# Performance work log

Measured on AMD Instinct MI355X. Metric: run time of the kernel, lower is better.

Reference implementation:

```python
import jax, jax.numpy as jnp
jax.config.update("jax_enable_x64", True)
import numpy as np

BATCH, N = 8192, 4096
EPS = 1e-6
NR_ITERS = 5  # Newton-Raphson iterations in the gate circuit


def setup_inputs() -> dict:
    key = jax.random.key(0)
    x = jax.random.normal(key, (BATCH, N), dtype=jnp.float32)
    return {"x": x}


def reference(x):
    # Faithful numeric emulation of the bit-pulse FP64 gate circuit.
    # The original encodes each scalar as 32 bit-pulses, widens to FP64,
    # and runs the exact arithmetic below on FP64 values, then narrows
    # back to FP32. We operate on the decoded floats directly.
    x64 = x.astype(jnp.float64)                      # FP32ToFP64Converter
    mean = jnp.mean(x64, axis=-1, keepdims=True)     # sum via FP64 adders / N
    c = x64 - mean                                   # x + (-mean) via sign NOT + adder
    var = jnp.mean(c * c, axis=-1, keepdims=True)    # FP64 squares, summed, / N
    vpe = var + EPS
    # rsqrt via Newton-Raphson, seeded with y0 = 1/(var+eps) (FP64 divider)
    y = 1.0 / vpe
    for _ in range(NR_ITERS):
        y = 0.5 * y * (3.0 - vpe * (y * y))
    out = c * y                                      # normalize
    return out.astype(jnp.float32)                   # FP64ToFP32Converter
```

## Files before the change

### kernel.cpp

```cpp
#include <hip/hip_runtime.h>


#define LN_BATCH 8192
#define LN_N     4096
#define LN_THREADS 256
#define LN_EPS 1e-6

__global__ __launch_bounds__(LN_THREADS)
void spike_layernorm_kernel(const float* __restrict__ x, float* __restrict__ out) {
    const int row  = blockIdx.x;
    const int t    = threadIdx.x;
    const int wave = t >> 6;
    const int lane = t & 63;

    const float4* __restrict__ xr  = reinterpret_cast<const float4*>(x + (size_t)row * LN_N);
    float4* __restrict__       orow = reinterpret_cast<float4*>(out + (size_t)row * LN_N);

    float4 v[4];
#pragma unroll
    for (int i = 0; i < 4; ++i) v[i] = xr[t + i * LN_THREADS];

    double s = 0.0;
#pragma unroll
    for (int i = 0; i < 4; ++i)
        s += (double)v[i].x + (double)v[i].y + (double)v[i].z + (double)v[i].w;

#pragma unroll
    for (int off = 32; off > 0; off >>= 1) s += __shfl_down(s, off, 64);

    __shared__ double red[4];
    __shared__ double bcast[2];
    if (lane == 0) red[wave] = s;
    __syncthreads();
    if (t == 0) {
        double tot = red[0] + red[1] + red[2] + red[3];
        bcast[0] = tot * (1.0 / LN_N);
    }
    __syncthreads();
    const double mean = bcast[0];

    double ss = 0.0;
#pragma unroll
    for (int i = 0; i < 4; ++i) {
        double d;
        d = (double)v[i].x - mean; ss += d * d;
        d = (double)v[i].y - mean; ss += d * d;
        d = (double)v[i].z - mean; ss += d * d;
        d = (double)v[i].w - mean; ss += d * d;
    }
#pragma unroll
    for (int off = 32; off > 0; off >>= 1) ss += __shfl_down(ss, off, 64);

    if (lane == 0) red[wave] = ss;
    __syncthreads();
    if (t == 0) {
        double var = (red[0] + red[1] + red[2] + red[3]) * (1.0 / LN_N);
        double vpe = var + LN_EPS;
        double y = 1.0 / vpe;
#pragma unroll
        for (int it = 0; it < 5; ++it)
            y = 0.5 * y * (3.0 - vpe * (y * y));
        bcast[1] = y;
    }
    __syncthreads();
    const double y = bcast[1];

#pragma unroll
    for (int i = 0; i < 4; ++i) {
        float4 o;
        o.x = (float)(((double)v[i].x - mean) * y);
        o.y = (float)(((double)v[i].y - mean) * y);
        o.z = (float)(((double)v[i].z - mean) * y);
        o.w = (float)(((double)v[i].w - mean) * y);
        orow[t + i * LN_THREADS] = o;
    }
}

extern "C" void kernel_launch(void* const* d_in, const int* in_sizes, int n_in,
                              void* d_out, int out_size, void* d_ws, size_t ws_size,
                              hipStream_t stream) {
    const float* x = (const float*)d_in[0];
    float* out = (float*)d_out;
    spike_layernorm_kernel<<<LN_BATCH, LN_THREADS, 0, stream>>>(x, out);
}
```

Before: 226.2 us.

## Map one wavefront per row with shuffle reductions and nontemporal accesses

Reassigns work so each 64-lane wave owns a whole row and holds 16 float4 values per lane, packing four rows per block. This removes all block-level barriers and shared-memory reductions in favor of xor-shuffle allreduces, and splits the FP64 accumulations into four independent chains. Loads and stores use nontemporal hints to avoid cache pollution on streaming data. The cost is higher register pressure per thread, which may reduce occupancy.

```diff
diff --git a/kernel.cpp b/kernel.cpp
--- a/kernel.cpp
+++ b/kernel.cpp
@@ -3,76 +3,83 @@
 
 #define LN_BATCH 8192
 #define LN_N     4096
-#define LN_THREADS 256
-#define LN_EPS 1e-6
+#define LN_WPB   4
+#define LN_THREADS (LN_WPB * 64)
+#define LN_F4PT  16
+#define LN_EPS   1e-6
+
+typedef float vfloat4 __attribute__((ext_vector_type(4)));
+
+__device__ __forceinline__ double wave_allreduce_add(double s) {
+#pragma unroll
+    for (int off = 1; off < 64; off <<= 1)
+        s += __shfl_xor(s, off, 64);
+    return s;
+}
 
 __global__ __launch_bounds__(LN_THREADS)
 void spike_layernorm_kernel(const float* __restrict__ x, float* __restrict__ out) {
-    const int row  = blockIdx.x;
-    const int t    = threadIdx.x;
-    const int wave = t >> 6;
-    const int lane = t & 63;
+    const int wave = threadIdx.x >> 6;
+    const int lane = threadIdx.x & 63;
+    const int row  = blockIdx.x * LN_WPB + wave;
 
-    const float4* __restrict__ xr  = reinterpret_cast<const float4*>(x + (size_t)row * LN_N);
-    float4* __restrict__       orow = reinterpret_cast<float4*>(out + (size_t)row * LN_N);
+    const vfloat4* __restrict__ xr =
+        reinterpret_cast<const vfloat4*>(x + (size_t)row * LN_N);
+    vfloat4* __restrict__ orow =
+        reinterpret_cast<vfloat4*>(out + (size_t)row * LN_N);
 
-    float4 v[4];
+    vfloat4 v[LN_F4PT];
 #pragma unroll
-    for (int i = 0; i < 4; ++i) v[i] = xr[t + i * LN_THREADS];
+    for (int i = 0; i < LN_F4PT; ++i)
+        v[i] = __builtin_nontemporal_load(&xr[lane + i * 64]);
 
-    double s = 0.0;
+    double s0 = 0.0, s1 = 0.0, s2 = 0.0, s3 = 0.0;
 #pragma unroll
-    for (int i = 0; i < 4; ++i)
-        s += (double)v[i].x + (double)v[i].y + (double)v[i].z + (double)v[i].w;
+    for (int i = 0; i < LN_F4PT; i += 4) {
+        s0 += (double)v[i + 0].x + (double)v[i + 0].y + (double)v[i + 0].z + (double)v[i + 0].w;
+        s1 += (double)v[i + 1].x + (double)v[i + 1].y + (double)v[i + 1].z + (double)v[i + 1].w;
+        s2 += (double)v[i + 2].x + (double)v[i + 2].y + (double)v[i + 2].z + (double)v[i + 2].w;
+        s3 += (double)v[i + 3].x + (double)v[i + 3].y + (double)v[i + 3].z + (double)v[i + 3].w;
+    }
+    const double mean = wave_allreduce_add((s0 + s1) + (s2 + s3)) * (1.0 / LN_N);
+
+    double q0 = 0.0, q1 = 0.0, q2 = 0.0, q3 = 0.0;
+#pragma unroll
+    for (int i = 0; i < LN_F4PT; i += 4) {
+        double d;
+        d = (double)v[i + 0].x - mean; q0 += d * d;
+        d = (double)v[i + 0].y - mean; q0 += d * d;
+        d = (double)v[i + 0].z - mean; q0 += d * d;
+        d = (double)v[i + 0].w - mean; q0 += d * d;
+        d = (double)v[i + 1].x - mean; q1 += d * d;
+        d = (double)v[i + 1].y - mean; q1 += d * d;
+        d = (double)v[i + 1].z - mean; q1 += d * d;
+        d = (double)v[i + 1].w - mean; q1 += d * d;
+        d = (double)v[i + 2].x - mean; q2 += d * d;
+        d = (double)v[i + 2].y - mean; q2 += d * d;
+        d = (double)v[i + 2].z - mean; q2 += d * d;
+        d = (double)v[i + 2].w - mean; q2 += d * d;
+        d = (double)v[i + 3].x - mean; q3 += d * d;
+        d = (double)v[i + 3].y - mean; q3 += d * d;
+        d = (double)v[i + 3].z - mean; q3 += d * d;
+        d = (double)v[i + 3].w - mean; q3 += d * d;
+    }
+    const double var = wave_allreduce_add((q0 + q1) + (q2 + q3)) * (1.0 / LN_N);
+
+    const double vpe = var + LN_EPS;
+    double y = 1.0 / vpe;
+#pragma unroll
+    for (int it = 0; it < 5; ++it)
+        y = 0.5 * y * (3.0 - vpe * (y * y));
 
 #pragma unroll
-    for (int off = 32; off > 0; off >>= 1) s += __shfl_down(s, off, 64);
-
-    __shared__ double red[4];
-    __shared__ double bcast[2];
-    if (lane == 0) red[wave] = s;
-    __syncthreads();
-    if (t == 0) {
-        double tot = red[0] + red[1] + red[2] + red[3];
-        bcast[0] = tot * (1.0 / LN_N);
-    }
-    __syncthreads();
-    const double mean = bcast[0];
-
-    double ss = 0.0;
-#pragma unroll
-    for (int i = 0; i < 4; ++i) {
-        double d;
-        d = (double)v[i].x - mean; ss += d * d;
-        d = (double)v[i].y - mean; ss += d * d;
-        d = (double)v[i].z - mean; ss += d * d;
-        d = (double)v[i].w - mean; ss += d * d;
-    }
-#pragma unroll
-    for (int off = 32; off > 0; off >>= 1) ss += __shfl_down(ss, off, 64);
-
-    if (lane == 0) red[wave] = ss;
-    __syncthreads();
-    if (t == 0) {
-        double var = (red[0] + red[1] + red[2] + red[3]) * (1.0 / LN_N);
-        double vpe = var + LN_EPS;
-        double y = 1.0 / vpe;
-#pragma unroll
-        for (int it = 0; it < 5; ++it)
-            y = 0.5 * y * (3.0 - vpe * (y * y));
-        bcast[1] = y;
-    }
-    __syncthreads();
-    const double y = bcast[1];
-
-#pragma unroll
-    for (int i = 0; i < 4; ++i) {
-        float4 o;
+    for (int i = 0; i < LN_F4PT; ++i) {
+        vfloat4 o;
         o.x = (float)(((double)v[i].x - mean) * y);
         o.y = (float)(((double)v[i].y - mean) * y);
         o.z = (float)(((double)v[i].z - mean) * y);
         o.w = (float)(((double)v[i].w - mean) * y);
-        orow[t + i * LN_THREADS] = o;
+        __builtin_nontemporal_store(o, &orow[lane + i * 64]);
     }
 }
 
@@ -81,5 +88,5 @@
                               hipStream_t stream) {
     const float* x = (const float*)d_in[0];
     float* out = (float*)d_out;
-    spike_layernorm_kernel<<<LN_BATCH, LN_THREADS, 0, stream>>>(x, out);
+    spike_layernorm_kernel<<<LN_BATCH / LN_WPB, LN_THREADS, 0, stream>>>(x, out);
 }
```

Measured after the change: 220.7 us. 2.4% less time.
